# Kernel tuning notes

Measured on AMD Instinct MI355X. Metric: run time of the kernel, lower is better.

## Reference

```python
import jax, jax.numpy as jnp
import numpy as np

C = 64
RED = 4            # attention reduction: conv_match C -> C//RED
CR = C // RED      # 16, also MultiScaleSpatialAttention reduced channels
N_HASHES = 4
CHUNK = 512
RES_SCALE = 0.1
EPS = 5e-5


def conv2d(x, w, b=None, padding=0, groups=1):
    out = jax.lax.conv_general_dilated(
        x, w, (1, 1), [(padding, padding), (padding, padding)],
        dimension_numbers=('NCHW', 'OIHW', 'NCHW'), feature_group_count=groups)
    if b is not None:
        out = out + b[None, :, None, None]
    return out


def ds_conv(x, pw_w, dw_w, dw_b, padding):
    # pointwise (no bias) then depthwise (bias)
    x = conv2d(x, pw_w)
    return conv2d(x, dw_w, dw_b, padding=padding, groups=dw_w.shape[0])


def pool2(x, mode):
    B, Cc, H, W = x.shape
    xr = x.reshape(B, Cc, H // 2, 2, W // 2, 2)
    return xr.max(axis=(3, 5)) if mode == 'max' else xr.mean(axis=(3, 5))


def bilinear_ac(x, out_h, out_w):
    # bilinear interpolation with align_corners=True (matches F.interpolate)
    B, Cc, h, w = x.shape
    def coords(n_in, n_out):
        pos = jnp.arange(n_out, dtype=x.dtype) * ((n_in - 1) / (n_out - 1))
        lo = jnp.floor(pos).astype(jnp.int32)
        hi = jnp.minimum(lo + 1, n_in - 1)
        frac = pos - lo.astype(x.dtype)
        return lo, hi, frac
    lo_h, hi_h, fh = coords(h, out_h)
    x = x[:, :, lo_h, :] * (1 - fh)[None, None, :, None] + x[:, :, hi_h, :] * fh[None, None, :, None]
    lo_w, hi_w, fw = coords(w, out_w)
    x = x[:, :, :, lo_w] * (1 - fw) + x[:, :, :, hi_w] * fw
    return x


def sparse_attn(x, wm, bm, wa, ba, rot):
    # NLSN-style LSH-chunked non-local sparse attention
    N, Cc, H, W = x.shape
    L = H * W
    xe = conv2d(x, wm, bm).reshape(N, -1, L).transpose(0, 2, 1)   # [N,L,Ce]
    ye = conv2d(x, wa, ba).reshape(N, -1, L).transpose(0, 2, 1)   # [N,L,C]
    Ce = xe.shape[-1]
    n_chunks = L // CHUNK                     # L multiple of CHUNK here -> no padding
    buckets = min(n_chunks + n_chunks % 2, 128)
    # LSH hashing (rot: [Ce, n_hashes, buckets//2])
    rv = jnp.einsum('blf,fhi->bhli', xe, rot)
    rv = jnp.concatenate([rv, -rv], axis=-1)  # [N,nh,L,buckets]
    codes = jnp.argmax(rv, axis=-1) + (jnp.arange(N_HASHES) * buckets)[None, :, None]
    codes = codes.reshape(N, -1)              # [N, nh*L]
    idx = jnp.argsort(codes, axis=-1)
    undo = jnp.argsort(idx, axis=-1)
    mod_idx = idx % L
    xs = jnp.take_along_axis(xe, mod_idx[:, :, None], axis=1)     # [N,nh*L,Ce]
    ys = jnp.take_along_axis(ye, mod_idx[:, :, None], axis=1)     # [N,nh*L,C]
    xb = xs.reshape(N, N_HASHES, n_chunks, CHUNK, Ce)
    yb = ys.reshape(N, N_HASHES, n_chunks, CHUNK, Cc)
    xm = xb / jnp.maximum(jnp.linalg.norm(xb, axis=-1, keepdims=True), EPS)
    def adj(t):  # add previous / next bucket (circular)
        return jnp.concatenate([t, jnp.roll(t, 1, axis=2), jnp.roll(t, -1, axis=2)], axis=3)
    xm3, yb3 = adj(xm), adj(yb)
    raw = jnp.einsum('bhkie,bhkje->bhkij', xb, xm3)               # [N,nh,k,CHUNK,3*CHUNK]
    bscore = jax.nn.logsumexp(raw, axis=-1, keepdims=True)
    score = jnp.exp(raw - bscore)
    ret = jnp.einsum('bhkij,bhkje->bhkie', score, yb3)            # [N,nh,k,CHUNK,C]
    ret = ret.reshape(N, N_HASHES * L, Cc)
    bscore = bscore.reshape(N, N_HASHES * L)
    ret = jnp.take_along_axis(ret, undo[:, :, None], axis=1).reshape(N, N_HASHES, L, Cc)
    bscore = jnp.take_along_axis(bscore, undo, axis=1).reshape(N, N_HASHES, L, 1)
    probs = jax.nn.softmax(bscore, axis=1)                        # over hash rounds
    out = (ret * probs).sum(axis=1)                               # [N,L,C]
    out = out.transpose(0, 2, 1).reshape(N, Cc, H, W)
    return out * RES_SCALE + x


def setup_inputs() -> dict:
    key = jax.random.key(0)
    ks = iter(jax.random.split(key, 40))
    w = lambda *s: jax.random.normal(next(ks), s, jnp.float32) * 0.1
    inp = {
        'x': jax.random.normal(next(ks), (2, C, 128, 128), jnp.float32),
        'spa_down_w': w(CR, C, 1, 1), 'spa_down_b': w(CR),
        's0_pw_w': w(2 * CR, CR, 1, 1), 's0_dw_w': w(2 * CR, 1, 1, 1), 's0_dw_b': w(2 * CR),
        'br3_pw_w': w(CR, CR, 1, 1), 'br3_dw_w': w(CR, 1, 3, 3), 'br3_dw_b': w(CR),
        'br5_pw_w': w(CR, CR, 1, 1), 'br5_dw_w': w(CR, 1, 5, 5), 'br5_dw_b': w(CR),
        'br7_pw_w': w(CR, CR, 1, 1), 'br7_dw_w': w(CR, 1, 7, 7), 'br7_dw_b': w(CR),
        'fusion_w': w(C, 8 * CR, 1, 1), 'fusion_b': w(C),
        'resid_w': w(C, C, 1, 1), 'resid_b': w(C),
        'ca_w1': w(C // 16, C, 1, 1), 'ca_b1': w(C // 16),
        'ca_w2': w(C, C // 16, 1, 1), 'ca_b2': w(C),
        'conv1x1_w': w(C, C, 1, 1), 'conv1x1_b': w(C),
        'match_w': w(CR, C, 1, 1), 'match_b': w(CR),
        'asm_w': w(C, C, 1, 1), 'asm_b': w(C),
        'rot': jax.random.normal(next(ks), (CR, N_HASHES, 16), jnp.float32),  # buckets//2 = 16
        'collect_w': w(C, C, 1, 1), 'collect_b': w(C),
    }
    return inp


def reference(x, spa_down_w, spa_down_b, s0_pw_w, s0_dw_w, s0_dw_b,
              br3_pw_w, br3_dw_w, br3_dw_b, br5_pw_w, br5_dw_w, br5_dw_b,
              br7_pw_w, br7_dw_w, br7_dw_b, fusion_w, fusion_b,
              resid_w, resid_b, ca_w1, ca_b1, ca_w2, ca_b2,
              conv1x1_w, conv1x1_b, match_w, match_b, asm_w, asm_b, rot,
              collect_w, collect_b):
    B, Cc, H, W = x.shape
    # --- MultiScaleSpatialAttention ---
    xr = conv2d(x, spa_down_w, spa_down_b)                # [B,16,H,W]
    s0 = ds_conv(xr, s0_pw_w, s0_dw_w, s0_dw_b, padding=0)
    feats = [s0]
    for pw, dw, db, pad in ((br3_pw_w, br3_dw_w, br3_dw_b, 1),
                            (br5_pw_w, br5_dw_w, br5_dw_b, 2),
                            (br7_pw_w, br7_dw_w, br7_dw_b, 3)):
        mx = ds_conv(pool2(xr, 'max'), pw, dw, db, pad)
        av = ds_conv(pool2(xr, 'avg'), pw, dw, db, pad)
        feats.append(jnp.concatenate([bilinear_ac(mx, H, W), bilinear_ac(av, H, W)], axis=1))
    attn = jax.nn.sigmoid(conv2d(jnp.concatenate(feats, axis=1), fusion_w, fusion_b))
    spa_mask = x * attn + conv2d(x, resid_w, resid_b)
    # --- CALayer ---
    y = x.mean(axis=(2, 3), keepdims=True)
    y = jax.nn.sigmoid(conv2d(jax.nn.relu(conv2d(y, ca_w1, ca_b1)), ca_w2, ca_b2))
    spe_mask = x * y
    # --- combine + SparseMaskConv (n_layers=1: attention then 1x1 collect) ---
    mask = conv2d(spa_mask + spe_mask, conv1x1_w, conv1x1_b) + x
    fea = sparse_attn(mask, match_w, match_b, asm_w, asm_b, rot)
    out1 = conv2d(fea, collect_w, collect_b)
    return out1 + x
```

## Files before the change

### kernel.cpp

```cpp
#include <hip/hip_runtime.h>
#include <math.h>

static constexpr int NB = 2;
static constexpr int NC = 64;
static constexpr int NHp = 128, NWp = 128;
static constexpr int NL = NHp * NWp;
static constexpr int NCR = 16;
static constexpr int NL2 = 64 * 64;
static constexpr int NHASH = 4;
static constexpr int CHUNKSZ = 512;
static constexpr int NCHUNKS = 32;
static constexpr int TOT = NHASH * NL;
static constexpr int NKEY = 128;
static constexpr int NTILE = 256;
static constexpr int TILESZ = TOT / NTILE;

typedef _Float16 half4 __attribute__((ext_vector_type(4)));
typedef _Float16 half8 __attribute__((ext_vector_type(8)));
typedef float f32x4 __attribute__((ext_vector_type(4)));

static constexpr size_t OFF_MASK = 0;
static constexpr size_t OFF_FEA  = OFF_MASK + (size_t)NB*NC*NL;
static constexpr size_t OFF_XE   = OFF_FEA  + (size_t)NB*NC*NL;
static constexpr size_t OFF_XEH  = OFF_XE   + (size_t)NB*NL*NCR;
static constexpr size_t OFF_XENH = OFF_XEH  + (size_t)NB*NL*NCR/2;
static constexpr size_t OFF_YEH  = OFF_XENH + (size_t)NB*NL*NCR/2;
static constexpr size_t OFF_RET  = OFF_YEH  + (size_t)NB*NL*NC/2;
static constexpr size_t OFF_BSC  = OFF_RET  + (size_t)NB*TOT*NC/2;
static constexpr size_t OFF_INT  = OFF_BSC  + (size_t)NB*TOT;
static constexpr size_t IOFF_CODES = 0;
static constexpr size_t IOFF_IDX   = IOFF_CODES + (size_t)NB*TOT;
static constexpr size_t IOFF_UNDO  = IOFF_IDX   + (size_t)NB*TOT;
static constexpr size_t IOFF_HIST  = IOFF_UNDO  + (size_t)NB*TOT;
static constexpr size_t IOFF_OFFS  = IOFF_HIST  + (size_t)NB*NKEY*NTILE/2;
static constexpr size_t IOFF_END   = IOFF_OFFS  + (size_t)NB*NKEY*NTILE/2;
static constexpr size_t OFF_CAY = OFF_INT + IOFF_END;
static constexpr size_t OFF_CAS = OFF_CAY + 128;
static constexpr size_t OFF_CRW = OFF_CAS + 128;
static constexpr size_t OFF_CRB = OFF_CRW + 4096;
static constexpr size_t OFF_PMX   = OFF_FEA;
static constexpr size_t OFF_PAV   = OFF_PMX  + (size_t)NB*NCR*NL2;
static constexpr size_t OFF_PTMP  = OFF_PAV  + (size_t)NB*NCR*NL2;
static constexpr size_t OFF_DWT   = OFF_PTMP + (size_t)6*NB*NCR*NL2;
static_assert(OFF_DWT + (size_t)6*NB*NCR*NL2 <= OFF_XE, "halfres overlay fits");
static constexpr size_t OFF_XR    = OFF_XE;
static constexpr size_t OFF_FEATS = OFF_XR + (size_t)NB*NCR*NL;
static_assert(OFF_FEATS + (size_t)NB*128*NL <= OFF_BSC, "feats overlay fits");
static constexpr size_t OFF_PRE1  = OFF_FEA;

__device__ __forceinline__ float sigmoidf_(float v){ return 1.0f/(1.0f + expf(-v)); }


__global__ __launch_bounds__(256,4) void k_xr(const float* __restrict__ x,
                     const float* __restrict__ w,
                     const float* __restrict__ b, float* __restrict__ xr){
  int gid = blockIdx.x*256 + threadIdx.x;
  int pix = gid >> 1, hf = gid & 1;
  int bb = pix >> 14, p = pix & (NL-1);
  const float* xi = x + (size_t)bb*NC*NL + (size_t)hf*32*NL + p;
  float acc[16];
  #pragma unroll
  for (int oc=0; oc<16; ++oc) acc[oc] = hf ? 0.f : b[oc];
  for (int ic0=0; ic0<32; ic0+=16){
    float r[16];
    #pragma unroll
    for (int j=0; j<16; ++j) r[j] = xi[(size_t)(ic0+j)*NL];
    #pragma unroll
    for (int oc=0; oc<16; ++oc){
      #pragma unroll
      for (int j=0; j<16; ++j) acc[oc] += r[j]*w[oc*64 + hf*32 + ic0 + j];
    }
  }
  #pragma unroll
  for (int oc=0; oc<16; ++oc) acc[oc] += __shfl_xor(acc[oc], 1, 64);
  if (!hf){
    float* xo = xr + (size_t)bb*NCR*NL + p;
    #pragma unroll
    for (int oc=0; oc<16; ++oc) xo[(size_t)oc*NL] = acc[oc];
  }
}

__global__ __launch_bounds__(256,4) void k_s0(const float* __restrict__ xr,
                     const float* __restrict__ pw,
                     const float* __restrict__ dww, const float* __restrict__ dwb,
                     float* __restrict__ feats){
  int gid = blockIdx.x*256 + threadIdx.x;
  int oc0 = blockIdx.y*16;
  int bb = gid >> 14, p = gid & (NL-1);
  const float* xi = xr + (size_t)bb*NCR*NL + p;
  float r[16];
  #pragma unroll
  for (int ic=0; ic<16; ++ic) r[ic] = xi[(size_t)ic*NL];
  float* fo = feats + (size_t)bb*128*NL + p;
  #pragma unroll
  for (int j=0; j<16; ++j){
    int oc = oc0 + j;
    float s = 0.f;
    #pragma unroll
    for (int ic=0; ic<16; ++ic) s += r[ic]*pw[oc*16+ic];
    fo[(size_t)oc*NL] = s*dww[oc] + dwb[oc];
  }
}

__global__ void k_pool(const float* __restrict__ xr, float* __restrict__ pmax,
                       float* __restrict__ pavg){
  int gid = blockIdx.x*256 + threadIdx.x;
  if (gid >= NB*NCR*NL2) return;
  int p = gid & (NL2-1); int t = gid >> 12; int c = t & 15; int bb = t >> 4;
  int y = p >> 6, x2 = p & 63;
  const float* base = xr + (size_t)(bb*NCR + c)*NL + (size_t)(2*y)*NWp + 2*x2;
  float a = base[0], b_ = base[1], c_ = base[NWp], d = base[NWp+1];
  pmax[gid] = fmaxf(fmaxf(a,b_), fmaxf(c_,d));
  pavg[gid] = 0.25f*(a+b_+c_+d);
}

__global__ void k_pw16_all(const float* __restrict__ pmx, const float* __restrict__ pav,
                           const float* __restrict__ w0, const float* __restrict__ w1,
                           const float* __restrict__ w2, float* __restrict__ out){
  int gid = blockIdx.x*256 + threadIdx.x;
  if (gid >= 6*NB*NL2) return;
  int p = gid & (NL2-1); int t = gid >> 12; int bb = t & 1; int combo = t >> 1;
  int br = combo >> 1, mode = combo & 1;
  const float* w = (br==0) ? w0 : (br==1) ? w1 : w2;
  const float* in = ((mode==0) ? pmx : pav) + (size_t)bb*NCR*NL2 + p;
  float r[16];
  #pragma unroll
  for (int ic=0; ic<16; ++ic) r[ic] = in[(size_t)ic*NL2];
  float* oo = out + ((size_t)(combo*NB + bb)*NCR)*NL2 + p;
  #pragma unroll
  for (int oc=0; oc<16; ++oc){
    float s = 0.f;
    #pragma unroll
    for (int ic=0; ic<16; ++ic) s += r[ic]*w[oc*16+ic];
    oo[(size_t)oc*NL2] = s;
  }
}

__global__ void k_dw_all(const float* __restrict__ in,
                         const float* __restrict__ w3, const float* __restrict__ b3,
                         const float* __restrict__ w5, const float* __restrict__ b5,
                         const float* __restrict__ w7, const float* __restrict__ b7,
                         float* __restrict__ out){
  int gid = blockIdx.x*256 + threadIdx.x;
  if (gid >= 6*NB*NCR*NL2) return;
  int p = gid & (NL2-1); int t = gid >> 12; int c = t & 15; int r2 = t >> 4;
  int bb = r2 & 1; int combo = r2 >> 1;
  int br = combo >> 1;
  int K = (br==0) ? 3 : (br==1) ? 5 : 7; int P = K >> 1;
  const float* w = (br==0) ? w3 : (br==1) ? w5 : w7;
  const float* bias = (br==0) ? b3 : (br==1) ? b5 : b7;
  int y = p >> 6, x = p & 63;
  const float* xi = in + ((size_t)(combo*NB + bb)*NCR + c)*NL2;
  float s = bias[c];
  for (int dy=0; dy<K; ++dy){
    int iy = y + dy - P;
    if ((unsigned)iy < 64u){
      for (int dx=0; dx<K; ++dx){
        int ix = x + dx - P;
        if ((unsigned)ix < 64u) s += xi[iy*64 + ix] * w[(c*K + dy)*K + dx];
      }
    }
  }
  out[gid] = s;
}

__global__ void k_up_all(const float* __restrict__ in, float* __restrict__ feats){
  int gid = blockIdx.x*256 + threadIdx.x;
  if (gid >= 6*NB*NCR*NL) return;
  int p = gid & (NL-1); int t = gid >> 14; int c = t & 15; int r2 = t >> 4;
  int bb = r2 & 1; int combo = r2 >> 1;
  int y = p >> 7, x = p & 127;
  const float sc = 63.0f/127.0f;
  float fy = y*sc; int ly = (int)floorf(fy); int hy = min(ly+1, 63); fy -= (float)ly;
  float fx = x*sc; int lx = (int)floorf(fx); int hx = min(lx+1, 63); float gx = fx - (float)lx;
  const float* xi = in + ((size_t)(combo*NB + bb)*NCR + c)*NL2;
  float v0 = xi[ly*64+lx]*(1.f-fy) + xi[hy*64+lx]*fy;
  float v1 = xi[ly*64+hx]*(1.f-fy) + xi[hy*64+hx]*fy;
  int coff = 32 + combo*16 + c;
  feats[(size_t)bb*128*NL + (size_t)coff*NL + p] = v0*(1.f-gx) + v1*gx;
}

__global__ void k_camean(const float* __restrict__ x, float* __restrict__ cay){
  __shared__ float red[256];
  int bc = blockIdx.x; int tid = threadIdx.x;
  float s = 0.f;
  for (int i = tid; i < NL; i += 256) s += x[(size_t)bc*NL + i];
  red[tid] = s; __syncthreads();
  for (int st=128; st>0; st>>=1){ if (tid<st) red[tid]+=red[tid+st]; __syncthreads(); }
  if (tid==0) cay[bc] = red[0] / (float)NL;
}

__global__ void k_camlp(const float* __restrict__ cay,
                        const float* __restrict__ w1, const float* __restrict__ b1,
                        const float* __restrict__ w2, const float* __restrict__ b2,
                        float* __restrict__ cas){
  __shared__ float z[NB*4];
  int tid = threadIdx.x;
  if (tid < NB*4){
    int bb = tid >> 2, j = tid & 3;
    float s = b1[j];
    for (int ic=0; ic<NC; ++ic) s += cay[bb*NC+ic]*w1[j*NC+ic];
    z[tid] = fmaxf(s, 0.f);
  }
  __syncthreads();
  if (tid < NB*NC){
    int bb = tid >> 6, oc = tid & 63;
    float s = b2[oc];
    #pragma unroll
    for (int j=0; j<4; ++j) s += z[bb*4+j]*w2[oc*4+j];
    cas[tid] = sigmoidf_(s);
  }
}

__global__ void k_wprod(const float* __restrict__ c11w, const float* __restrict__ c11b,
                        const float* __restrict__ rw, const float* __restrict__ rb,
                        float* __restrict__ crw, float* __restrict__ crb){
  int gid = blockIdx.x*256 + threadIdx.x;
  if (gid >= 4096) return;
  int o = gid >> 6, i = gid & 63;
  float s = 0.f;
  for (int k=0; k<64; ++k) s += c11w[o*64+k]*rw[k*64+i];
  crw[gid] = s;
  if (i == 0){
    float t = c11b[o];
    for (int k=0; k<64; ++k) t += c11w[o*64+k]*rb[k];
    crb[o] = t;
  }
}

__global__ __launch_bounds__(256,4) void k_attnmul(const float* __restrict__ x,
                          const float* __restrict__ feats,
                          const float* __restrict__ fw, const float* __restrict__ fb,
                          const float* __restrict__ cas, float* __restrict__ pre1){
  int gid = blockIdx.x*256 + threadIdx.x;
  int oc0 = blockIdx.y*16;
  int bb = gid >> 14, p = gid & (NL-1);
  const float* fi = feats + (size_t)bb*128*NL + p;
  float acc[16];
  #pragma unroll
  for (int j=0; j<16; ++j) acc[j] = fb[oc0+j];
  for (int k0=0; k0<128; k0+=8){
    float fr[8];
    #pragma unroll
    for (int j=0; j<8; ++j) fr[j] = fi[(size_t)(k0+j)*NL];
    #pragma unroll
    for (int j=0; j<16; ++j){
      #pragma unroll
      for (int t=0; t<8; ++t) acc[j] += fr[t]*fw[(oc0+j)*128+k0+t];
    }
  }
  const float* xb = x + (size_t)bb*NC*NL + p;
  float* po = pre1 + (size_t)bb*NC*NL + p;
  #pragma unroll
  for (int j=0; j<16; ++j){
    int oc = oc0 + j;
    float xv = xb[(size_t)oc*NL];
    po[(size_t)oc*NL] = xv*(sigmoidf_(acc[j]) + cas[bb*64+oc]);
  }
}

__global__ __launch_bounds__(256,4) void k_mask(const float* __restrict__ pre1,
                       const float* __restrict__ c11w,
                       const float* __restrict__ crw, const float* __restrict__ crb,
                       const float* __restrict__ x, float* __restrict__ mask){
  int gid = blockIdx.x*256 + threadIdx.x;
  int oc0 = blockIdx.y*16;
  int bb = gid >> 14, p = gid & (NL-1);
  const float* pi = pre1 + (size_t)bb*NC*NL + p;
  const float* xi = x + (size_t)bb*NC*NL + p;
  float acc[16];
  #pragma unroll
  for (int j=0; j<16; ++j) acc[j] = crb[oc0+j];
  for (int ic0=0; ic0<64; ic0+=8){
    float pr[8], xr8[8];
    #pragma unroll
    for (int j=0; j<8; ++j){ pr[j] = pi[(size_t)(ic0+j)*NL]; xr8[j] = xi[(size_t)(ic0+j)*NL]; }
    #pragma unroll
    for (int j=0; j<16; ++j){
      #pragma unroll
      for (int t=0; t<8; ++t)
        acc[j] += pr[t]*c11w[(oc0+j)*64+ic0+t] + xr8[t]*crw[(oc0+j)*64+ic0+t];
    }
  }
  float* mo = mask + (size_t)bb*NC*NL + p;
  #pragma unroll
  for (int j=0; j<16; ++j){
    int oc = oc0 + j;
    mo[(size_t)oc*NL] = acc[j] + xi[(size_t)oc*NL];
  }
}


__global__ __launch_bounds__(256,4) void k_xe(const float* __restrict__ mask,
                     const float* __restrict__ w,
                     const float* __restrict__ b, float* __restrict__ xe,
                     _Float16* __restrict__ xeh, _Float16* __restrict__ xenh){
  int gid = blockIdx.x*256 + threadIdx.x;
  int pix = gid >> 1, hf = gid & 1;
  int bb = pix >> 14, l = pix & (NL-1);
  const float* mi = mask + (size_t)bb*NC*NL + (size_t)hf*32*NL + l;
  float acc[16];
  #pragma unroll
  for (int oc=0; oc<16; ++oc) acc[oc] = hf ? 0.f : b[oc];
  for (int ic0=0; ic0<32; ic0+=16){
    float r[16];
    #pragma unroll
    for (int j=0; j<16; ++j) r[j] = mi[(size_t)(ic0+j)*NL];
    #pragma unroll
    for (int oc=0; oc<16; ++oc){
      #pragma unroll
      for (int j=0; j<16; ++j) acc[oc] += r[j]*w[oc*64 + hf*32 + ic0 + j];
    }
  }
  #pragma unroll
  for (int oc=0; oc<16; ++oc) acc[oc] += __shfl_xor(acc[oc], 1, 64);
  if (!hf){
    float n2 = 0.f;
    #pragma unroll
    for (int oc=0; oc<16; ++oc) n2 += acc[oc]*acc[oc];
    float inv = 1.0f / fmaxf(sqrtf(n2), 5e-5f);
    float* xo = xe + (size_t)pix*NCR;
    _Float16* ho = xeh + (size_t)pix*NCR;
    _Float16* no = xenh + (size_t)pix*NCR;
    #pragma unroll
    for (int g=0; g<4; ++g){
      f32x4 v; half4 hv, nv;
      #pragma unroll
      for (int j=0; j<4; ++j){ v[j] = acc[g*4+j]; hv[j] = (_Float16)acc[g*4+j]; nv[j] = (_Float16)(acc[g*4+j]*inv); }
      *(f32x4*)(xo + g*4) = v;
      *(half4*)(ho + g*4) = hv;
      *(half4*)(no + g*4) = nv;
    }
  }
}

__global__ __launch_bounds__(256,4) void k_yeh(const float* __restrict__ mask,
                      const float* __restrict__ w,
                      const float* __restrict__ b, _Float16* __restrict__ yeh){
  int gid = blockIdx.x*256 + threadIdx.x;
  int oc0 = blockIdx.y*16;
  int bb = gid >> 14, l = gid & (NL-1);
  const float* mi = mask + (size_t)bb*NC*NL + l;
  float acc[16];
  #pragma unroll
  for (int j=0; j<16; ++j) acc[j] = b[oc0+j];
  for (int ic0=0; ic0<64; ic0+=8){
    float r[8];
    #pragma unroll
    for (int j=0; j<8; ++j) r[j] = mi[(size_t)(ic0+j)*NL];
    #pragma unroll
    for (int j=0; j<16; ++j){
      #pragma unroll
      for (int t=0; t<8; ++t) acc[j] += r[t]*w[(oc0+j)*64+ic0+t];
    }
  }
  _Float16* yo = yeh + (size_t)(bb*NL + l)*NC + oc0;
  #pragma unroll
  for (int g=0; g<2; ++g){
    half8 h;
    #pragma unroll
    for (int j=0; j<8; ++j) h[j] = (_Float16)acc[g*8+j];
    *(half8*)(yo + g*8) = h;
  }
}

__global__ void k_codes(const float* __restrict__ xe, const float* __restrict__ rot,
                        int* __restrict__ codes){
  int gid = blockIdx.x*256 + threadIdx.x;
  if (gid >= NB*NHASH*NL) return;
  int l = gid & (NL-1); int t = gid >> 14; int h = t & 3; int bb = t >> 2;
  const float* v = xe + (size_t)(bb*NL + l)*NCR;
  float q[16];
  #pragma unroll
  for (int f=0; f<16; ++f) q[f] = v[f];
  float rv[16];
  #pragma unroll
  for (int i=0; i<16; ++i){
    float s = 0.f;
    #pragma unroll
    for (int f=0; f<16; ++f) s += q[f]*rot[(f*NHASH + h)*16 + i];
    rv[i] = s;
  }
  float best = -1e30f; int bi = 0;
  #pragma unroll
  for (int i=0; i<16; ++i){ if (rv[i] > best){ best = rv[i]; bi = i; } }
  #pragma unroll
  for (int i=0; i<16; ++i){ float val = -rv[i]; if (val > best){ best = val; bi = 16+i; } }
  codes[gid] = bi + h*32;
}

__global__ void k_zero(int* __restrict__ p, int n){
  int i = blockIdx.x*256 + threadIdx.x;
  if (i < n) p[i] = 0;
}

__global__ void k_hist(const int* __restrict__ codes, int* __restrict__ hist){
  __shared__ int h[NKEY];
  int bt = blockIdx.x; int bb = bt >> 8; int tile = bt & 255;
  int tid = threadIdx.x;
  h[tid] = 0; __syncthreads();
  for (int i = tid; i < TILESZ; i += 128)
    atomicAdd(&h[codes[bb*TOT + tile*TILESZ + i]], 1);
  __syncthreads();
  hist[bb*NKEY*NTILE + tid*NTILE + tile] = h[tid];
}

__global__ void k_scan(const int* __restrict__ hist, int* __restrict__ offs){
  __shared__ int part[256];
  int bb = blockIdx.x; int t = threadIdx.x;
  const int* hi = hist + (size_t)bb*NKEY*NTILE;
  int* oo = offs + (size_t)bb*NKEY*NTILE;
  int s = 0;
  for (int i=0; i<128; ++i) s += hi[t*128 + i];
  part[t] = s; __syncthreads();
  if (t == 0){ int acc = 0; for (int i=0;i<256;++i){ int v=part[i]; part[i]=acc; acc+=v; } }
  __syncthreads();
  int run = part[t];
  for (int i=0; i<128; ++i){ int v = hi[t*128+i]; oo[t*128+i] = run; run += v; }
}

__global__ void k_scatter(const int* __restrict__ codes, const int* __restrict__ offs,
                          int* __restrict__ idx, int* __restrict__ undo){
  __shared__ int cnt[NKEY];
  int tid = threadIdx.x;
  cnt[tid] = 0; __syncthreads();
  if (tid == 0){
    int bt = blockIdx.x; int bb = bt >> 8; int tile = bt & 255;
    const int* cb = codes + bb*TOT;
    const int* ob = offs + (size_t)bb*NKEY*NTILE;
    int* ib = idx + bb*TOT;
    int* ub = undo + bb*TOT;
    #pragma unroll 4
    for (int i=0; i<TILESZ; ++i){
      int j = tile*TILESZ + i;
      int k = cb[j];
      int pos = ob[k*NTILE + tile] + cnt[k]++;
      ib[pos] = j;
      ub[j] = pos;
    }
  }
}

__global__ __launch_bounds__(512) void k_attn(
    const _Float16* __restrict__ xeh, const _Float16* __restrict__ xenh,
    const _Float16* __restrict__ yeh, const int* __restrict__ idx,
    _Float16* __restrict__ retb, float* __restrict__ bsc){
  __shared__ _Float16 kt[64*24];
  __shared__ _Float16 vt[64*72];
  int blk = blockIdx.x;
  int kk = blk & 31; int h = (blk >> 5) & 3; int bb = blk >> 7;
  int tid = threadIdx.x;
  int w = tid >> 6, lane = tid & 63, col = lane & 15, grp = lane >> 4;
  const int* idxb = idx + bb*TOT;
  int qbase = h*NL + kk*CHUNKSZ + w*64;

  half4 qfr[4]; int posq[4];
  #pragma unroll
  for (int qf=0; qf<4; ++qf){
    posq[qf] = qbase + qf*16 + col;
    int lq = idxb[posq[qf]] & (NL-1);
    qfr[qf] = *(const half4*)(xeh + ((size_t)bb*NL + lq)*16 + grp*4);
  }

  f32x4 O[4][4];
  #pragma unroll
  for (int a=0; a<4; ++a)
    #pragma unroll
    for (int b=0; b<4; ++b) O[a][b] = (f32x4){0.f,0.f,0.f,0.f};
  float m_[4] = {-1e30f,-1e30f,-1e30f,-1e30f};
  float ssum[4] = {0.f,0.f,0.f,0.f};

  for (int t=0; t<24; ++t){
    __syncthreads();
    {
      int kx = tid & 63, c0 = (tid >> 6) * 8;
      int jj = t*64 + kx; int sec = jj >> 9; int j0 = jj & 511;
      int cc = kk + ((sec==1) ? -1 : (sec==2) ? 1 : 0);
      cc = (cc + NCHUNKS) & (NCHUNKS-1);
      int lv = idxb[h*NL + cc*CHUNKSZ + j0] & (NL-1);
      half8 vv = *(const half8*)(yeh + ((size_t)bb*NL + lv)*64 + c0);
      #pragma unroll
      for (int j=0; j<8; ++j) vt[(c0+j)*72 + kx] = vv[j];
    }
    if (tid < 128){
      int r = tid >> 1, hf = tid & 1;
      int jj = t*64 + r; int sec = jj >> 9; int j0 = jj & 511;
      int cc = kk + ((sec==1) ? -1 : (sec==2) ? 1 : 0);
      cc = (cc + NCHUNKS) & (NCHUNKS-1);
      int lk = idxb[h*NL + cc*CHUNKSZ + j0] & (NL-1);
      *(half8*)(kt + r*24 + hf*8) =
          *(const half8*)(xenh + ((size_t)bb*NL + lk)*16 + hf*8);
    }
    __syncthreads();

    f32x4 S[4][4];
    #pragma unroll
    for (int kb=0; kb<4; ++kb){
      half4 ka = *(const half4*)(kt + (kb*16 + col)*24 + grp*4);
      #pragma unroll
      for (int qf=0; qf<4; ++qf)
        S[kb][qf] = __builtin_amdgcn_mfma_f32_16x16x16f16(
            ka, qfr[qf], (f32x4){0.f,0.f,0.f,0.f}, 0, 0, 0);
    }

    half4 pf[4][4];
    #pragma unroll
    for (int qf=0; qf<4; ++qf){
      float mt = -1e30f;
      #pragma unroll
      for (int kb=0; kb<4; ++kb)
        #pragma unroll
        for (int i=0; i<4; ++i) mt = fmaxf(mt, S[kb][qf][i]);
      mt = fmaxf(mt, __shfl_xor(mt, 16, 64));
      mt = fmaxf(mt, __shfl_xor(mt, 32, 64));
      float mn = fmaxf(m_[qf], mt);
      float sc = __expf(m_[qf] - mn);
      float ps = 0.f;
      #pragma unroll
      for (int kb=0; kb<4; ++kb){
        #pragma unroll
        for (int i=0; i<4; ++i){
          float p = __expf(S[kb][qf][i] - mn);
          ps += p;
          pf[qf][kb][i] = (_Float16)p;
        }
      }
      ps += __shfl_xor(ps, 16, 64);
      ps += __shfl_xor(ps, 32, 64);
      ssum[qf] = ssum[qf]*sc + ps;
      m_[qf] = mn;
      #pragma unroll
      for (int cf=0; cf<4; ++cf)
        #pragma unroll
        for (int i=0; i<4; ++i) O[cf][qf][i] *= sc;
    }

    #pragma unroll
    for (int cf=0; cf<4; ++cf){
      #pragma unroll
      for (int kb=0; kb<4; ++kb){
        half4 va = *(const half4*)(vt + (cf*16 + col)*72 + kb*16 + grp*4);
        #pragma unroll
        for (int qf=0; qf<4; ++qf)
          O[cf][qf] = __builtin_amdgcn_mfma_f32_16x16x16f16(
              va, pf[qf][kb], O[cf][qf], 0, 0, 0);
      }
    }
  }

  #pragma unroll
  for (int qf=0; qf<4; ++qf){
    float inv = 1.0f/ssum[qf];
    size_t rb = ((size_t)bb*TOT + posq[qf])*64;
    #pragma unroll
    for (int cf=0; cf<4; ++cf){
      half4 o;
      #pragma unroll
      for (int i=0; i<4; ++i) o[i] = (_Float16)(O[cf][qf][i]*inv);
      *(half4*)(retb + rb + cf*16 + grp*4) = o;
    }
    if (grp == 0) bsc[(size_t)bb*TOT + posq[qf]] = m_[qf] + logf(ssum[qf]);
  }
}

__global__ __launch_bounds__(256,4) void k_combine(const _Float16* __restrict__ retb,
                          const float* __restrict__ bsc,
                          const int* __restrict__ undo, const float* __restrict__ mask,
                          float* __restrict__ fea){
  int gid = blockIdx.x*256 + threadIdx.x;
  int c0 = blockIdx.y*32;
  int bb = gid >> 14; int l = gid & (NL-1);
  const int* ub = undo + bb*TOT;
  int pos[4]; float sc[4];
  #pragma unroll
  for (int h=0; h<4; ++h){ pos[h] = ub[h*NL + l]; sc[h] = bsc[bb*TOT + pos[h]]; }
  float mx = fmaxf(fmaxf(sc[0],sc[1]), fmaxf(sc[2],sc[3]));
  float e[4]; float tot = 0.f;
  #pragma unroll
  for (int h=0; h<4; ++h){ e[h] = __expf(sc[h]-mx); tot += e[h]; }
  float inv = 0.1f/tot;
  const float* mb_ = mask + (size_t)bb*NC*NL + l;
  float* fo = fea + (size_t)bb*NC*NL + l;
  const _Float16* r0 = retb + ((size_t)bb*TOT + pos[0])*NC + c0;
  const _Float16* r1 = retb + ((size_t)bb*TOT + pos[1])*NC + c0;
  const _Float16* r2 = retb + ((size_t)bb*TOT + pos[2])*NC + c0;
  const _Float16* r3 = retb + ((size_t)bb*TOT + pos[3])*NC + c0;
  #pragma unroll
  for (int g=0; g<4; ++g){
    half8 v0 = *(const half8*)(r0 + g*8);
    half8 v1 = *(const half8*)(r1 + g*8);
    half8 v2 = *(const half8*)(r2 + g*8);
    half8 v3 = *(const half8*)(r3 + g*8);
    #pragma unroll
    for (int j=0; j<8; ++j){
      int c = c0 + g*8 + j;
      float v = (float)v0[j]*e[0] + (float)v1[j]*e[1] + (float)v2[j]*e[2] + (float)v3[j]*e[3];
      fo[(size_t)c*NL] = v*inv + mb_[(size_t)c*NL];
    }
  }
}

__global__ __launch_bounds__(256,4) void k_collect(const float* __restrict__ fea,
                          const float* __restrict__ w,
                          const float* __restrict__ b, const float* __restrict__ x,
                          float* __restrict__ out){
  int gid = blockIdx.x*256 + threadIdx.x;
  int oc0 = blockIdx.y*16;
  int bb = gid >> 14, p = gid & (NL-1);
  const float* fi = fea + (size_t)bb*NC*NL + p;
  const float* xi = x + (size_t)bb*NC*NL + p;
  float acc[16];
  #pragma unroll
  for (int j=0; j<16; ++j) acc[j] = b[oc0+j];
  for (int ic0=0; ic0<64; ic0+=8){
    float r[8];
    #pragma unroll
    for (int j=0; j<8; ++j) r[j] = fi[(size_t)(ic0+j)*NL];
    #pragma unroll
    for (int j=0; j<16; ++j){
      #pragma unroll
      for (int t=0; t<8; ++t) acc[j] += r[t]*w[(oc0+j)*64+ic0+t];
    }
  }
  float* oo = out + (size_t)bb*NC*NL + p;
  #pragma unroll
  for (int j=0; j<16; ++j){
    int oc = oc0 + j;
    oo[(size_t)oc*NL] = acc[j] + xi[(size_t)oc*NL];
  }
}

extern "C" void kernel_launch(void* const* d_in, const int* in_sizes, int n_in,
                              void* d_out, int out_size, void* d_ws, size_t ws_size,
                              hipStream_t stream) {
  const float* x        = (const float*)d_in[0];
  const float* spa_dw   = (const float*)d_in[1];
  const float* spa_db   = (const float*)d_in[2];
  const float* s0_pw    = (const float*)d_in[3];
  const float* s0_dww   = (const float*)d_in[4];
  const float* s0_dwb   = (const float*)d_in[5];
  const float* fus_w    = (const float*)d_in[15];
  const float* fus_b    = (const float*)d_in[16];
  const float* res_w    = (const float*)d_in[17];
  const float* res_b    = (const float*)d_in[18];
  const float* ca_w1    = (const float*)d_in[19];
  const float* ca_b1    = (const float*)d_in[20];
  const float* ca_w2    = (const float*)d_in[21];
  const float* ca_b2    = (const float*)d_in[22];
  const float* c11_w    = (const float*)d_in[23];
  const float* c11_b    = (const float*)d_in[24];
  const float* match_w  = (const float*)d_in[25];
  const float* match_b  = (const float*)d_in[26];
  const float* asm_w    = (const float*)d_in[27];
  const float* asm_b    = (const float*)d_in[28];
  const float* rot      = (const float*)d_in[29];
  const float* col_w    = (const float*)d_in[30];
  const float* col_b    = (const float*)d_in[31];
  float* out = (float*)d_out;

  float* ws    = (float*)d_ws;
  float* mask  = ws + OFF_MASK;
  float* fea   = ws + OFF_FEA;
  float* xe    = ws + OFF_XE;
  _Float16* xeh  = (_Float16*)(ws + OFF_XEH);
  _Float16* xenh = (_Float16*)(ws + OFF_XENH);
  _Float16* yeh  = (_Float16*)(ws + OFF_YEH);
  _Float16* retb = (_Float16*)(ws + OFF_RET);
  float* bsc   = ws + OFF_BSC;
  int*   ib    = (int*)(ws + OFF_INT);
  int* codes   = ib + IOFF_CODES;
  int* idx     = ib + IOFF_IDX;
  int* undo    = ib + IOFF_UNDO;
  int* hist    = ib + IOFF_HIST;
  int* offs    = ib + IOFF_OFFS;
  float* cay   = ws + OFF_CAY;
  float* cas   = ws + OFF_CAS;
  float* crw   = ws + OFF_CRW;
  float* crb   = ws + OFF_CRB;
  float* xr    = ws + OFF_XR;
  float* feats = ws + OFF_FEATS;
  float* pmx   = ws + OFF_PMX;
  float* pav   = ws + OFF_PAV;
  float* ptmp  = ws + OFF_PTMP;
  float* dwt   = ws + OFF_DWT;
  float* pre1  = ws + OFF_PRE1;

  k_xr<<<(NB*NL*2)/256, 256, 0, stream>>>(x, spa_dw, spa_db, xr);
  k_wprod<<<16, 256, 0, stream>>>(c11_w, c11_b, res_w, res_b, crw, crb);
  k_s0<<<dim3((NB*NL)/256, 2), 256, 0, stream>>>(xr, s0_pw, s0_dww, s0_dwb, feats);
  k_pool<<<(NB*NCR*NL2)/256, 256, 0, stream>>>(xr, pmx, pav);
  k_pw16_all<<<(6*NB*NL2)/256, 256, 0, stream>>>(pmx, pav,
      (const float*)d_in[6], (const float*)d_in[9], (const float*)d_in[12], ptmp);
  k_dw_all<<<(6*NB*NCR*NL2)/256, 256, 0, stream>>>(ptmp,
      (const float*)d_in[7], (const float*)d_in[8],
      (const float*)d_in[10], (const float*)d_in[11],
      (const float*)d_in[13], (const float*)d_in[14], dwt);
  k_up_all<<<(6*NB*NCR*NL)/256, 256, 0, stream>>>(dwt, feats);
  k_camean<<<NB*NC, 256, 0, stream>>>(x, cay);
  k_camlp<<<1, 128, 0, stream>>>(cay, ca_w1, ca_b1, ca_w2, ca_b2, cas);
  k_attnmul<<<dim3((NB*NL)/256, 4), 256, 0, stream>>>(x, feats, fus_w, fus_b, cas, pre1);
  k_mask<<<dim3((NB*NL)/256, 4), 256, 0, stream>>>(pre1, c11_w, crw, crb, x, mask);

  k_xe<<<(NB*NL*2)/256, 256, 0, stream>>>(mask, match_w, match_b, xe, xeh, xenh);
  k_yeh<<<dim3((NB*NL)/256, 4), 256, 0, stream>>>(mask, asm_w, asm_b, yeh);
  k_codes<<<(NB*NHASH*NL)/256, 256, 0, stream>>>(xe, rot, codes);
  k_zero<<<(NB*NKEY*NTILE + 255)/256, 256, 0, stream>>>(hist, NB*NKEY*NTILE);
  k_hist<<<NB*NTILE, 128, 0, stream>>>(codes, hist);
  k_scan<<<NB, 256, 0, stream>>>(hist, offs);
  k_scatter<<<NB*NTILE, 128, 0, stream>>>(codes, offs, idx, undo);
  k_attn<<<NB*NHASH*NCHUNKS, 512, 0, stream>>>(xeh, xenh, yeh, idx, retb, bsc);
  k_combine<<<dim3((NB*NL)/256, 2), 256, 0, stream>>>(retb, bsc, undo, mask, fea);
  k_collect<<<dim3((NB*NL)/256, 4), 256, 0, stream>>>(fea, col_w, col_b, x, out);
}
```

Measured before the change: 348.6 us.

## Fuse LSH code computation into xe kernel, split attention blocks, add lazy softmax rescale

```diff
diff --git a/kernel.cpp b/kernel.cpp
--- a/kernel.cpp
+++ b/kernel.cpp
@@ -292,9 +292,10 @@
 
 
 __global__ __launch_bounds__(256,4) void k_xe(const float* __restrict__ mask,
-                     const float* __restrict__ w,
-                     const float* __restrict__ b, float* __restrict__ xe,
-                     _Float16* __restrict__ xeh, _Float16* __restrict__ xenh){
+                     const float* __restrict__ w, const float* __restrict__ b,
+                     const float* __restrict__ rot,
+                     _Float16* __restrict__ xeh, _Float16* __restrict__ xenh,
+                     int* __restrict__ codes){
   int gid = blockIdx.x*256 + threadIdx.x;
   int pix = gid >> 1, hf = gid & 1;
   int bb = pix >> 14, l = pix & (NL-1);
@@ -319,18 +320,34 @@
     #pragma unroll
     for (int oc=0; oc<16; ++oc) n2 += acc[oc]*acc[oc];
     float inv = 1.0f / fmaxf(sqrtf(n2), 5e-5f);
-    float* xo = xe + (size_t)pix*NCR;
     _Float16* ho = xeh + (size_t)pix*NCR;
     _Float16* no = xenh + (size_t)pix*NCR;
     #pragma unroll
     for (int g=0; g<4; ++g){
-      f32x4 v; half4 hv, nv;
-      #pragma unroll
-      for (int j=0; j<4; ++j){ v[j] = acc[g*4+j]; hv[j] = (_Float16)acc[g*4+j]; nv[j] = (_Float16)(acc[g*4+j]*inv); }
-      *(f32x4*)(xo + g*4) = v;
+      half4 hv, nv;
+      #pragma unroll
+      for (int j=0; j<4; ++j){ hv[j] = (_Float16)acc[g*4+j]; nv[j] = (_Float16)(acc[g*4+j]*inv); }
       *(half4*)(ho + g*4) = hv;
       *(half4*)(no + g*4) = nv;
     }
+  }
+  #pragma unroll
+  for (int hh=0; hh<2; ++hh){
+    int h = hf*2 + hh;
+    float rv[16];
+    #pragma unroll
+    for (int i=0; i<16; ++i){
+      float s = 0.f;
+      #pragma unroll
+      for (int f=0; f<16; ++f) s += acc[f]*rot[(f*NHASH + h)*16 + i];
+      rv[i] = s;
+    }
+    float best = -1e30f; int bi = 0;
+    #pragma unroll
+    for (int i=0; i<16; ++i){ if (rv[i] > best){ best = rv[i]; bi = i; } }
+    #pragma unroll
+    for (int i=0; i<16; ++i){ float val = -rv[i]; if (val > best){ best = val; bi = 16+i; } }
+    codes[((bb*NHASH + h) << 14) + l] = bi + h*32;
   }
 }
 
@@ -362,36 +379,6 @@
     for (int j=0; j<8; ++j) h[j] = (_Float16)acc[g*8+j];
     *(half8*)(yo + g*8) = h;
   }
-}
-
-__global__ void k_codes(const float* __restrict__ xe, const float* __restrict__ rot,
-                        int* __restrict__ codes){
-  int gid = blockIdx.x*256 + threadIdx.x;
-  if (gid >= NB*NHASH*NL) return;
-  int l = gid & (NL-1); int t = gid >> 14; int h = t & 3; int bb = t >> 2;
-  const float* v = xe + (size_t)(bb*NL + l)*NCR;
-  float q[16];
-  #pragma unroll
-  for (int f=0; f<16; ++f) q[f] = v[f];
-  float rv[16];
-  #pragma unroll
-  for (int i=0; i<16; ++i){
-    float s = 0.f;
-    #pragma unroll
-    for (int f=0; f<16; ++f) s += q[f]*rot[(f*NHASH + h)*16 + i];
-    rv[i] = s;
-  }
-  float best = -1e30f; int bi = 0;
-  #pragma unroll
-  for (int i=0; i<16; ++i){ if (rv[i] > best){ best = rv[i]; bi = i; } }
-  #pragma unroll
-  for (int i=0; i<16; ++i){ float val = -rv[i]; if (val > best){ best = val; bi = 16+i; } }
-  codes[gid] = bi + h*32;
-}
-
-__global__ void k_zero(int* __restrict__ p, int n){
-  int i = blockIdx.x*256 + threadIdx.x;
-  if (i < n) p[i] = 0;
 }
 
 __global__ void k_hist(const int* __restrict__ codes, int* __restrict__ hist){
@@ -441,18 +428,18 @@
   }
 }
 
-__global__ __launch_bounds__(512) void k_attn(
+__global__ __launch_bounds__(256,4) void k_attn(
     const _Float16* __restrict__ xeh, const _Float16* __restrict__ xenh,
     const _Float16* __restrict__ yeh, const int* __restrict__ idx,
     _Float16* __restrict__ retb, float* __restrict__ bsc){
   __shared__ _Float16 kt[64*24];
   __shared__ _Float16 vt[64*72];
   int blk = blockIdx.x;
-  int kk = blk & 31; int h = (blk >> 5) & 3; int bb = blk >> 7;
+  int qh = blk & 1; int kk = (blk >> 1) & 31; int h = (blk >> 6) & 3; int bb = blk >> 8;
   int tid = threadIdx.x;
   int w = tid >> 6, lane = tid & 63, col = lane & 15, grp = lane >> 4;
   const int* idxb = idx + bb*TOT;
-  int qbase = h*NL + kk*CHUNKSZ + w*64;
+  int qbase = h*NL + kk*CHUNKSZ + qh*256 + w*64;
 
   half4 qfr[4]; int posq[4];
   #pragma unroll
@@ -473,14 +460,18 @@
   for (int t=0; t<24; ++t){
     __syncthreads();
     {
-      int kx = tid & 63, c0 = (tid >> 6) * 8;
+      int kx = tid & 63, c0 = (tid >> 6) * 16;
       int jj = t*64 + kx; int sec = jj >> 9; int j0 = jj & 511;
       int cc = kk + ((sec==1) ? -1 : (sec==2) ? 1 : 0);
       cc = (cc + NCHUNKS) & (NCHUNKS-1);
       int lv = idxb[h*NL + cc*CHUNKSZ + j0] & (NL-1);
-      half8 vv = *(const half8*)(yeh + ((size_t)bb*NL + lv)*64 + c0);
-      #pragma unroll
-      for (int j=0; j<8; ++j) vt[(c0+j)*72 + kx] = vv[j];
+      const _Float16* yp = yeh + ((size_t)bb*NL + lv)*64;
+      half8 vv0 = *(const half8*)(yp + c0);
+      half8 vv1 = *(const half8*)(yp + c0 + 8);
+      #pragma unroll
+      for (int j=0; j<8; ++j) vt[(c0+j)*72 + kx] = vv0[j];
+      #pragma unroll
+      for (int j=0; j<8; ++j) vt[(c0+8+j)*72 + kx] = vv1[j];
     }
     if (tid < 128){
       int r = tid >> 1, hf = tid & 1;
@@ -513,26 +504,29 @@
         for (int i=0; i<4; ++i) mt = fmaxf(mt, S[kb][qf][i]);
       mt = fmaxf(mt, __shfl_xor(mt, 16, 64));
       mt = fmaxf(mt, __shfl_xor(mt, 32, 64));
-      float mn = fmaxf(m_[qf], mt);
-      float sc = __expf(m_[qf] - mn);
+      if (__any(mt > m_[qf] + 8.0f)){
+        float mn = fmaxf(m_[qf], mt);
+        float sc = __expf(m_[qf] - mn);
+        ssum[qf] *= sc;
+        m_[qf] = mn;
+        #pragma unroll
+        for (int cf=0; cf<4; ++cf)
+          #pragma unroll
+          for (int i=0; i<4; ++i) O[cf][qf][i] *= sc;
+      }
       float ps = 0.f;
       #pragma unroll
       for (int kb=0; kb<4; ++kb){
         #pragma unroll
         for (int i=0; i<4; ++i){
-          float p = __expf(S[kb][qf][i] - mn);
+          float p = __expf(S[kb][qf][i] - m_[qf]);
           ps += p;
           pf[qf][kb][i] = (_Float16)p;
         }
       }
       ps += __shfl_xor(ps, 16, 64);
       ps += __shfl_xor(ps, 32, 64);
-      ssum[qf] = ssum[qf]*sc + ps;
-      m_[qf] = mn;
-      #pragma unroll
-      for (int cf=0; cf<4; ++cf)
-        #pragma unroll
-        for (int i=0; i<4; ++i) O[cf][qf][i] *= sc;
+      ssum[qf] += ps;
     }
 
     #pragma unroll
@@ -661,7 +655,6 @@
   float* ws    = (float*)d_ws;
   float* mask  = ws + OFF_MASK;
   float* fea   = ws + OFF_FEA;
-  float* xe    = ws + OFF_XE;
   _Float16* xeh  = (_Float16*)(ws + OFF_XEH);
   _Float16* xenh = (_Float16*)(ws + OFF_XENH);
   _Float16* yeh  = (_Float16*)(ws + OFF_YEH);
@@ -701,14 +694,12 @@
   k_attnmul<<<dim3((NB*NL)/256, 4), 256, 0, stream>>>(x, feats, fus_w, fus_b, cas, pre1);
   k_mask<<<dim3((NB*NL)/256, 4), 256, 0, stream>>>(pre1, c11_w, crw, crb, x, mask);
 
-  k_xe<<<(NB*NL*2)/256, 256, 0, stream>>>(mask, match_w, match_b, xe, xeh, xenh);
+  k_xe<<<(NB*NL*2)/256, 256, 0, stream>>>(mask, match_w, match_b, rot, xeh, xenh, codes);
   k_yeh<<<dim3((NB*NL)/256, 4), 256, 0, stream>>>(mask, asm_w, asm_b, yeh);
-  k_codes<<<(NB*NHASH*NL)/256, 256, 0, stream>>>(xe, rot, codes);
-  k_zero<<<(NB*NKEY*NTILE + 255)/256, 256, 0, stream>>>(hist, NB*NKEY*NTILE);
   k_hist<<<NB*NTILE, 128, 0, stream>>>(codes, hist);
   k_scan<<<NB, 256, 0, stream>>>(hist, offs);
   k_scatter<<<NB*NTILE, 128, 0, stream>>>(codes, offs, idx, undo);
-  k_attn<<<NB*NHASH*NCHUNKS, 512, 0, stream>>>(xeh, xenh, yeh, idx, retb, bsc);
+  k_attn<<<NB*NHASH*NCHUNKS*2, 256, 0, stream>>>(xeh, xenh, yeh, idx, retb, bsc);
   k_combine<<<dim3((NB*NL)/256, 2), 256, 0, stream>>>(retb, bsc, undo, mask, fea);
   k_collect<<<dim3((NB*NL)/256, 4), 256, 0, stream>>>(fea, col_w, col_b, x, out);
 }
```

Result: slower. 490.5 us (+40.7%).
